# Optimization experiments

Measured on AMD Instinct MI355X. Metric: run time of the kernel, lower is better.

## Reference

```python
import jax, jax.numpy as jnp
import numpy as np
import math

_DENSE_LOCAL_W = 64
_DYADIC = [96, 128, 192, 256, 384, 512, 768, 1024, 1536]
OFFSETS = sorted(set(range(0, _DENSE_LOCAL_W + 1)) | set(_DYADIC))  # 74 offsets

B, N, D, H = 1, 2048, 1024, 16
HD = D // H


def setup_inputs() -> dict:
    key = jax.random.key(0)
    ks = jax.random.split(key, 8)
    s = 1.0 / math.sqrt(D)
    x = jax.random.normal(ks[0], (B, N, D), dtype=jnp.float32)
    Wqkv = jax.random.uniform(ks[1], (3 * D, D), jnp.float32, -s, s)
    bqkv = jax.random.uniform(ks[2], (3 * D,), jnp.float32, -s, s)
    Wgate = jax.random.uniform(ks[3], (D, D), jnp.float32, -s, s)
    bgate = jax.random.uniform(ks[4], (D,), jnp.float32, -s, s)
    Wout = jax.random.uniform(ks[5], (D, D), jnp.float32, -s, s)
    bout = jax.random.uniform(ks[6], (D,), jnp.float32, -s, s)
    # pos_bias init exactly as in the module: -log(1+delta) * alpha_h, shape (O, H)
    alphas = jnp.linspace(0.2, 2.0, H)
    deltas = jnp.array([math.log(1.0 + d) for d in OFFSETS], dtype=jnp.float32)
    pos_bias = -deltas[:, None] * alphas[None, :]
    offsets = jnp.array(OFFSETS, dtype=jnp.int32)
    return {"x": x, "Wqkv": Wqkv, "bqkv": bqkv, "Wgate": Wgate, "bgate": bgate,
            "Wout": Wout, "bout": bout, "pos_bias": pos_bias, "offsets": offsets}


def reference(x, Wqkv, bqkv, Wgate, bgate, Wout, bout, pos_bias, offsets):
    Bx, Nx, Dx = x.shape
    qkv = x @ Wqkv.T + bqkv                       # (B, N, 3D)
    q, k, v = jnp.split(qkv, 3, axis=-1)
    q = q.reshape(Bx, Nx, H, HD).transpose(0, 2, 1, 3)  # (B, H, N, HD)
    k = k.reshape(Bx, Nx, H, HD).transpose(0, 2, 1, 3)
    v = v.reshape(Bx, Nx, H, HD).transpose(0, 2, 1, 3)
    scale = HD ** -0.5

    # gather shifted K/V: position n attends to n - delta for each fixed offset
    n_idx = jnp.arange(Nx, dtype=jnp.int32)[:, None]      # (N, 1)
    idx = n_idx - offsets[None, :]                        # (N, O)
    valid = idx >= 0                                      # (N, O)
    idx_c = jnp.clip(idx, 0, Nx - 1)
    K_all = k[:, :, idx_c, :]                             # (B, H, N, O, HD)
    V_all = v[:, :, idx_c, :]

    scores = jnp.einsum('bhnd,bhnod->bhno', q, K_all) * scale
    scores = scores + pos_bias.T[None, :, None, :]        # (1, H, 1, O)
    scores = jnp.where(valid[None, None], scores, -jnp.inf)
    alpha = jax.nn.softmax(scores, axis=-1)               # (B, H, N, O)
    out = jnp.einsum('bhno,bhnod->bhnd', alpha, V_all)    # (B, H, N, HD)

    flat = out.transpose(0, 2, 1, 3).reshape(Bx, Nx, Dx)  # (B, N, D)
    gate = jax.nn.sigmoid(x @ Wgate.T + bgate)
    return (flat * gate) @ Wout.T + bout                  # dropout = identity (eval)
```

## Files before the change

### kernel.cpp

```cpp
#include <hip/hip_runtime.h>
#include <hip/hip_bf16.h>

#define SEQ_N 2048
#define DIM   1024
#define NHEAD 16
#define HDIM  64
#define LDQ   4096
#define NOFF  74
#define NDENSE 65
#define NJ    224
#define NT    16
#define PST   232
#define QST   88

typedef __attribute__((ext_vector_type(8)))  __bf16 bv8;
typedef __attribute__((ext_vector_type(4)))  __bf16 bv4;
typedef __attribute__((ext_vector_type(4)))  float  f32x4;
typedef __attribute__((ext_vector_type(16))) float  f32x16;

typedef __attribute__((address_space(3))) void as3_void;
typedef __attribute__((address_space(1))) void as1_void;

__device__ __forceinline__ void async16(const void* g, void* l) {
  __builtin_amdgcn_global_load_lds((as1_void*)(unsigned long long)g,
                                   (as3_void*)l, 16, 0, 0);
}

#define E1 (SEQ_N * DIM)
#define E2 (E1 + 3 * DIM * DIM)
#define E3 (E2 + DIM * DIM)
#define E4 (E3 + DIM * DIM)
__global__ __launch_bounds__(256) void cvt_all(
    const float* __restrict__ x, const float* __restrict__ wqkv,
    const float* __restrict__ wgate, const float* __restrict__ wout,
    __bf16* __restrict__ dst) {
  long i = ((long)blockIdx.x * 256 + threadIdx.x) * 8;
  if (i >= E4) return;
  const float* s; long o;
  if (i < E1)      { s = x;     o = i; }
  else if (i < E2) { s = wqkv;  o = i - E1; }
  else if (i < E3) { s = wgate; o = i - E2; }
  else             { s = wout;  o = i - E3; }
  float4 v0 = *(const float4*)(s + o);
  float4 v1 = *(const float4*)(s + o + 4);
  bv8 ov;
  ov[0] = (__bf16)v0.x; ov[1] = (__bf16)v0.y; ov[2] = (__bf16)v0.z; ov[3] = (__bf16)v0.w;
  ov[4] = (__bf16)v1.x; ov[5] = (__bf16)v1.y; ov[6] = (__bf16)v1.z; ov[7] = (__bf16)v1.w;
  *(bv8*)(dst + i) = ov;
}

#define BM 128
#define BKT 128

template <int BN_, typename OutT>
__global__ __launch_bounds__(256) void gemm_bt(
    const __bf16* __restrict__ A, const __bf16* __restrict__ B1,
    const __bf16* __restrict__ B2, const float* __restrict__ bias1,
    const float* __restrict__ bias2, int Nsplit,
    OutT* __restrict__ C, int ldc, int K) {
  __shared__ __attribute__((aligned(16))) __bf16 Asm[BM * BKT];
  __shared__ __attribute__((aligned(16))) __bf16 Bsm[BN_ * BKT];
  constexpr int NJ32 = BN_ / 64;
  constexpr int CA = BM * BKT / 8;
  constexpr int CB = BN_ * BKT / 8;
  constexpr int CPR = BKT / 8;

  const int tid  = threadIdx.x;
  const int lane = tid & 63;
  const int wave = tid >> 6;
  const int wr = wave >> 1, wc = wave & 1;
  const int m31 = lane & 31;
  const int h1  = lane >> 5;
  const int l7  = lane & 7;

  const int bn0 = blockIdx.x * BN_;
  const int bm0 = blockIdx.y * BM;

  const __bf16* Bp;
  const float* biasp;
  if (bn0 < Nsplit) { Bp = B1 + (size_t)bn0 * K;            biasp = bias1 + bn0; }
  else              { Bp = B2 + (size_t)(bn0 - Nsplit) * K; biasp = bias2 + (bn0 - Nsplit); }
  const __bf16* Ap = A + (size_t)bm0 * K;

  f32x16 acc[2][NJ32] = {};

  for (int kt = 0; kt < K; kt += BKT) {
    __syncthreads();
#pragma unroll
    for (int c0 = 0; c0 < CA + CB; c0 += 256) {
      int c = c0 + tid;
      if (c < CA) {
        int rr = c / CPR, qq = c % CPR;
        int qs = qq ^ (rr & 7);
        async16(Ap + (size_t)rr * K + kt + qs * 8, Asm + c * 8);
      } else {
        int cb = c - CA;
        int rr = cb / CPR, qq = cb % CPR;
        int qs = qq ^ (rr & 7);
        async16(Bp + (size_t)rr * K + kt + qs * 8, Bsm + cb * 8);
      }
    }
    __syncthreads();

#pragma unroll
    for (int kk = 0; kk < BKT / 16; ++kk) {
      const int qs = ((kk * 2 + h1) ^ l7) * 8;
      bv8 af[2], bfr[NJ32];
#pragma unroll
      for (int i = 0; i < 2; ++i)
        af[i] = *(const bv8*)(Asm + (wr * 64 + i * 32 + m31) * BKT + qs);
#pragma unroll
      for (int j = 0; j < NJ32; ++j)
        bfr[j] = *(const bv8*)(Bsm + (wc * (BN_ / 2) + j * 32 + m31) * BKT + qs);
#pragma unroll
      for (int i = 0; i < 2; ++i)
#pragma unroll
        for (int j = 0; j < NJ32; ++j)
          acc[i][j] = __builtin_amdgcn_mfma_f32_32x32x16_bf16(af[i], bfr[j], acc[i][j], 0, 0, 0);
    }
  }

#pragma unroll
  for (int i = 0; i < 2; ++i) {
#pragma unroll
    for (int j = 0; j < NJ32; ++j) {
      int ccol = wc * (BN_ / 2) + j * 32 + m31;
      float b = biasp[ccol];
#pragma unroll
      for (int reg = 0; reg < 16; ++reg) {
        int row = bm0 + wr * 64 + i * 32 + (reg & 3) + 8 * (reg >> 2) + 4 * h1;
        C[(size_t)row * ldc + bn0 + ccol] = (OutT)(acc[i][j][reg] + b);
      }
    }
  }
}

template <typename OutT>
__global__ __launch_bounds__(256) void gemm_bt64(
    const __bf16* __restrict__ A, const __bf16* __restrict__ B,
    const float* __restrict__ bias, OutT* __restrict__ C, int ldc, int K) {
  __shared__ __attribute__((aligned(16))) __bf16 Asm[64 * BKT];
  __shared__ __attribute__((aligned(16))) __bf16 Bsm[64 * BKT];
  constexpr int CM = 64 * BKT / 8;
  constexpr int CPR = BKT / 8;

  const int tid  = threadIdx.x;
  const int lane = tid & 63;
  const int wave = tid >> 6;
  const int wr = wave >> 1, wc = wave & 1;
  const int m31 = lane & 31;
  const int h1  = lane >> 5;
  const int l7  = lane & 7;

  const int bn0 = blockIdx.x * 64;
  const int bm0 = blockIdx.y * 64;

  const __bf16* Ap = A + (size_t)bm0 * K;
  const __bf16* Bp = B + (size_t)bn0 * K;
  const float* biasp = bias + bn0;

  f32x16 acc = {};

  for (int kt = 0; kt < K; kt += BKT) {
    __syncthreads();
#pragma unroll
    for (int c0 = 0; c0 < CM; c0 += 256) {
      int c = c0 + tid;
      int rr = c / CPR, qq = c % CPR;
      int qs = qq ^ (rr & 7);
      async16(Ap + (size_t)rr * K + kt + qs * 8, Asm + c * 8);
      async16(Bp + (size_t)rr * K + kt + qs * 8, Bsm + c * 8);
    }
    __syncthreads();

#pragma unroll
    for (int kk = 0; kk < BKT / 16; ++kk) {
      const int qs = ((kk * 2 + h1) ^ l7) * 8;
      bv8 a = *(const bv8*)(Asm + (wr * 32 + m31) * BKT + qs);
      bv8 b = *(const bv8*)(Bsm + (wc * 32 + m31) * BKT + qs);
      acc = __builtin_amdgcn_mfma_f32_32x32x16_bf16(a, b, acc, 0, 0, 0);
    }
  }

  {
    int ccol = wc * 32 + m31;
    float b = biasp[ccol];
#pragma unroll
    for (int reg = 0; reg < 16; ++reg) {
      int row = bm0 + wr * 32 + (reg & 3) + 8 * (reg >> 2) + 4 * h1;
      C[(size_t)row * ldc + bn0 + ccol] = (OutT)(acc[reg] + b);
    }
  }
}

__global__ __launch_bounds__(256) void attn_mfma(
    const __bf16* __restrict__ qkv,
    const float* __restrict__ pos_bias,
    const int* __restrict__ offsets,
    __bf16* __restrict__ fg) {
  const int n0 = (blockIdx.x >> 4) * NT;
  const int h  = blockIdx.x & 15;
  const int tid = threadIdx.x;
  const int lane = tid & 63;
  const int w = tid >> 6;
  const int fr = lane & 15, fq = lane >> 4;
  const int fr7 = fr & 7;

  __shared__ __attribute__((aligned(16))) __bf16 KVbuf[NJ * HDIM];
  __shared__ __attribute__((aligned(16))) __bf16 Qbuf[NT * QST];
  __shared__ __attribute__((aligned(16))) float  Sbuf[NT][80];
  __shared__ __attribute__((aligned(16))) __bf16 Pd[NT * PST];
  __shared__ float inv_l[NT];

  const int ch = lane & 7;
  const int rowin = lane >> 3;

  if (tid < 128) {
    int ni = tid >> 3, cq = tid & 7;
    bv8 q = *(const bv8*)(qkv + (size_t)(n0 + ni) * LDQ + h * HDIM + cq * 8);
    *(bv8*)(Qbuf + ni * QST + cq * 8) = q;
  }
#pragma unroll
  for (int c0 = 0; c0 < NT * PST / 8; c0 += 256) {
    int c = c0 + tid;
    if (c < NT * PST / 8) *(uint4*)(Pd + c * 8) = make_uint4(0, 0, 0, 0);
  }
  {
    int chs = ch ^ rowin;
#pragma unroll
    for (int it = 0; it < 7; ++it) {
      int jbase = it * 32 + w * 8;
      int j = jbase + rowin;
      int g;
      if (j < 80) g = n0 - 64 + j;
      else { int jj = j - 80; g = n0 - offsets[NDENSE + (jj >> 4)] + (jj & 15); }
      if (g < 0) g = 0;
      async16(qkv + (size_t)g * LDQ + DIM + h * HDIM + chs * 8,
              KVbuf + jbase * HDIM + lane * 8);
    }
  }
  __syncthreads();

  for (int jb = w; jb < 14; jb += 4) {
    f32x4 acc = {};
#pragma unroll
    for (int kk = 0; kk < 2; ++kk) {
      bv8 a = *(const bv8*)(Qbuf + fr * QST + kk * 32 + fq * 8);
      bv8 b = *(const bv8*)(KVbuf + (jb * 16 + fr) * HDIM + ((kk * 4 + fq) ^ fr7) * 8);
      acc = __builtin_amdgcn_mfma_f32_16x16x32_bf16(a, b, acc, 0, 0, 0);
    }
    int j = jb * 16 + fr;
    if (jb < 5) {
      bool gvalid = (n0 - 64 + j) >= 0;
#pragma unroll
      for (int r = 0; r < 4; ++r) {
        int ni = fq * 4 + r;
        int o = ni + 64 - j;
        if (o >= 0 && o < NDENSE)
          Sbuf[ni][o] = gvalid ? acc[r] : -3.0e38f;
      }
    } else {
      int jj = j - 80;
      int s = jj >> 4, tni = jj & 15;
      int r = tni - fq * 4;
      if (r >= 0 && r < 4) {
        bool gvalid = (n0 + tni - offsets[NDENSE + s]) >= 0;
        Sbuf[tni][NDENSE + s] = gvalid ? acc[r] : -3.0e38f;
      }
    }
  }
  __syncthreads();

  {
#pragma unroll
    for (int it = 0; it < 7; ++it) {
      int jbase = it * 32 + w * 8;
      int jv = jbase + (lane >> 5) * 4 + ((lane >> 1) & 3);
      int dv = ((lane >> 3) & 3) * 16 + (lane & 1) * 8;
      int g;
      if (jv < 80) g = n0 - 64 + jv;
      else { int jj = jv - 80; g = n0 - offsets[NDENSE + (jj >> 4)] + (jj & 15); }
      if (g < 0) g = 0;
      async16(qkv + (size_t)g * LDQ + 2 * DIM + h * HDIM + dv,
              KVbuf + jbase * HDIM + lane * 8);
    }
  }

  {
    int t = tid & 15, ni = tid >> 4;
    float sc5[5];
    float m = -3.0e38f;
#pragma unroll
    for (int k = 0; k < 5; ++k) {
      int o = t + k * 16;
      float v = -3.0e38f;
      if (o < NOFF) {
        float raw = Sbuf[ni][o];
        if (raw > -1.0e38f) v = raw * 0.125f + pos_bias[o * NHEAD + h];
      }
      sc5[k] = v;
      m = fmaxf(m, v);
    }
#pragma unroll
    for (int d = 1; d < 16; d <<= 1) m = fmaxf(m, __shfl_xor(m, d));
    float sum = 0.f;
#pragma unroll
    for (int k = 0; k < 5; ++k) {
      int o = t + k * 16;
      if (o < NOFF && sc5[k] > -1.0e38f) {
        float e = __expf(sc5[k] - m);
        sum += e;
        int j = (o < NDENSE) ? (ni + 64 - o) : (80 + (o - NDENSE) * 16 + ni);
        Pd[ni * PST + j] = (__bf16)e;
      }
    }
#pragma unroll
    for (int d = 1; d < 16; d <<= 1) sum += __shfl_xor(sum, d);
    if (t == 0) inv_l[ni] = 1.f / sum;
  }
  __syncthreads();

  {
    const int db = w;
    const unsigned vb0 = (unsigned)(size_t)(as3_void*)KVbuf
                       + fq * 1024 + db * 128 + fr * 8;
    f32x4 acc = {};
#pragma unroll
    for (int kt = 0; kt < 7; ++kt) {
      bv8 a = *(const bv8*)(Pd + fr * PST + kt * 32 + fq * 8);
      bv4 lo, hi;
      asm volatile("ds_read_b64_tr_b16 %0, %2 offset:%3\n\t"
                   "ds_read_b64_tr_b16 %1, %2 offset:%4\n\t"
                   "s_waitcnt lgkmcnt(0)"
                   : "=&v"(lo), "=&v"(hi)
                   : "v"(vb0), "i"(kt * 4096), "i"(kt * 4096 + 512));
      bv8 b;
#pragma unroll
      for (int jj = 0; jj < 4; ++jj) { b[jj] = lo[jj]; b[4 + jj] = hi[jj]; }
      acc = __builtin_amdgcn_mfma_f32_16x16x32_bf16(a, b, acc, 0, 0, 0);
    }
    int d = db * 16 + fr;
#pragma unroll
    for (int r = 0; r < 4; ++r) {
      int ni = fq * 4 + r;
      float o = acc[r] * inv_l[ni];
      float gp = (float)qkv[(size_t)(n0 + ni) * LDQ + 3 * DIM + h * HDIM + d];
      float gate = 1.f / (1.f + __expf(-gp));
      fg[(size_t)(n0 + ni) * DIM + h * HDIM + d] = (__bf16)(o * gate);
    }
  }
}

extern "C" void kernel_launch(void* const* d_in, const int* in_sizes, int n_in,
                              void* d_out, int out_size, void* d_ws, size_t ws_size,
                              hipStream_t stream) {
  const float* x        = (const float*)d_in[0];
  const float* Wqkv     = (const float*)d_in[1];
  const float* bqkv     = (const float*)d_in[2];
  const float* Wgate    = (const float*)d_in[3];
  const float* bgate    = (const float*)d_in[4];
  const float* Wout     = (const float*)d_in[5];
  const float* bout     = (const float*)d_in[6];
  const float* pos_bias = (const float*)d_in[7];
  const int*   offsets  = (const int*)d_in[8];
  float* out = (float*)d_out;

  __bf16* xb       = (__bf16*)d_ws;
  __bf16* Wqkvb    = xb    + (size_t)SEQ_N * DIM;
  __bf16* Wgateb   = Wqkvb + (size_t)3 * DIM * DIM;
  __bf16* Woutb    = Wgateb + (size_t)DIM * DIM;
  __bf16* qkvg     = Woutb + (size_t)DIM * DIM;
  __bf16* flatgate = qkvg + (size_t)SEQ_N * LDQ;

  cvt_all<<<dim3(E4 / 2048), dim3(256), 0, stream>>>(x, Wqkv, Wgate, Wout, xb);

  gemm_bt<128, __bf16><<<dim3(LDQ / 128, SEQ_N / BM), dim3(256), 0, stream>>>(
      xb, Wqkvb, Wgateb, bqkv, bgate, 3 * DIM, qkvg, LDQ, DIM);

  attn_mfma<<<dim3((SEQ_N / NT) * NHEAD), dim3(256), 0, stream>>>(
      qkvg, pos_bias, offsets, flatgate);

  gemm_bt64<float><<<dim3(DIM / 64, SEQ_N / 64), dim3(256), 0, stream>>>(
      flatgate, Woutb, bout, out, DIM, DIM);
}
```

Baseline: 142.9 us.

## Shrink QKV GEMM tiles, add occupancy hint, and remap blocks for XCD locality

Reworks the fused QKV/gate GEMM to use 64x128 tiles with a 64-deep K step, which gives 1024 workgroups instead of 512 and lets four blocks share a CU via launch bounds. Both GEMMs now remap the linear block id so that consecutive blocks on the same XCD (bid & 7) cover adjacent work tiles, with the aim of better L2 reuse of A and B rows. The price is more global-load and barrier iterations per output element and smaller per-block data reuse.

```diff
diff --git a/kernel.cpp b/kernel.cpp
--- a/kernel.cpp
+++ b/kernel.cpp
@@ -49,21 +49,19 @@
   *(bv8*)(dst + i) = ov;
 }
 
-#define BM 128
-#define BKT 128
-
-template <int BN_, typename OutT>
-__global__ __launch_bounds__(256) void gemm_bt(
+template <int BM_, int BN_, int KT, int GX, int GY, typename OutT>
+__global__ __launch_bounds__(256, 4) void gemm_bt(
     const __bf16* __restrict__ A, const __bf16* __restrict__ B1,
     const __bf16* __restrict__ B2, const float* __restrict__ bias1,
     const float* __restrict__ bias2, int Nsplit,
     OutT* __restrict__ C, int ldc, int K) {
-  __shared__ __attribute__((aligned(16))) __bf16 Asm[BM * BKT];
-  __shared__ __attribute__((aligned(16))) __bf16 Bsm[BN_ * BKT];
+  __shared__ __attribute__((aligned(16))) __bf16 Asm[BM_ * KT];
+  __shared__ __attribute__((aligned(16))) __bf16 Bsm[BN_ * KT];
+  constexpr int NI   = BM_ / 64;
   constexpr int NJ32 = BN_ / 64;
-  constexpr int CA = BM * BKT / 8;
-  constexpr int CB = BN_ * BKT / 8;
-  constexpr int CPR = BKT / 8;
+  constexpr int CA = BM_ * KT / 8;
+  constexpr int CB = BN_ * KT / 8;
+  constexpr int CPR = KT / 8;
 
   const int tid  = threadIdx.x;
   const int lane = tid & 63;
@@ -73,8 +71,11 @@
   const int h1  = lane >> 5;
   const int l7  = lane & 7;
 
-  const int bn0 = blockIdx.x * BN_;
-  const int bm0 = blockIdx.y * BM;
+  constexpr int NWG = GX * GY;
+  const int bid  = blockIdx.y * GX + blockIdx.x;
+  const int work = (bid & 7) * (NWG >> 3) + (bid >> 3);
+  const int bn0 = (work / GY) * BN_;
+  const int bm0 = (work % GY) * BM_;
 
   const __bf16* Bp;
   const float* biasp;
@@ -82,9 +83,9 @@
   else              { Bp = B2 + (size_t)(bn0 - Nsplit) * K; biasp = bias2 + (bn0 - Nsplit); }
   const __bf16* Ap = A + (size_t)bm0 * K;
 
-  f32x16 acc[2][NJ32] = {};
-
-  for (int kt = 0; kt < K; kt += BKT) {
+  f32x16 acc[NI][NJ32] = {};
+
+  for (int kt = 0; kt < K; kt += KT) {
     __syncthreads();
 #pragma unroll
     for (int c0 = 0; c0 < CA + CB; c0 += 256) {
@@ -103,17 +104,17 @@
     __syncthreads();
 
 #pragma unroll
-    for (int kk = 0; kk < BKT / 16; ++kk) {
+    for (int kk = 0; kk < KT / 16; ++kk) {
       const int qs = ((kk * 2 + h1) ^ l7) * 8;
-      bv8 af[2], bfr[NJ32];
-#pragma unroll
-      for (int i = 0; i < 2; ++i)
-        af[i] = *(const bv8*)(Asm + (wr * 64 + i * 32 + m31) * BKT + qs);
+      bv8 af[NI], bfr[NJ32];
+#pragma unroll
+      for (int i = 0; i < NI; ++i)
+        af[i] = *(const bv8*)(Asm + (wr * (BM_ / 2) + i * 32 + m31) * KT + qs);
 #pragma unroll
       for (int j = 0; j < NJ32; ++j)
-        bfr[j] = *(const bv8*)(Bsm + (wc * (BN_ / 2) + j * 32 + m31) * BKT + qs);
-#pragma unroll
-      for (int i = 0; i < 2; ++i)
+        bfr[j] = *(const bv8*)(Bsm + (wc * (BN_ / 2) + j * 32 + m31) * KT + qs);
+#pragma unroll
+      for (int i = 0; i < NI; ++i)
 #pragma unroll
         for (int j = 0; j < NJ32; ++j)
           acc[i][j] = __builtin_amdgcn_mfma_f32_32x32x16_bf16(af[i], bfr[j], acc[i][j], 0, 0, 0);
@@ -121,21 +122,23 @@
   }
 
 #pragma unroll
-  for (int i = 0; i < 2; ++i) {
+  for (int i = 0; i < NI; ++i) {
 #pragma unroll
     for (int j = 0; j < NJ32; ++j) {
       int ccol = wc * (BN_ / 2) + j * 32 + m31;
       float b = biasp[ccol];
 #pragma unroll
       for (int reg = 0; reg < 16; ++reg) {
-        int row = bm0 + wr * 64 + i * 32 + (reg & 3) + 8 * (reg >> 2) + 4 * h1;
+        int row = bm0 + wr * (BM_ / 2) + i * 32 + (reg & 3) + 8 * (reg >> 2) + 4 * h1;
         C[(size_t)row * ldc + bn0 + ccol] = (OutT)(acc[i][j][reg] + b);
       }
     }
   }
 }
 
-template <typename OutT>
+#define BKT 128
+
+template <int GX, int GY, typename OutT>
 __global__ __launch_bounds__(256) void gemm_bt64(
     const __bf16* __restrict__ A, const __bf16* __restrict__ B,
     const float* __restrict__ bias, OutT* __restrict__ C, int ldc, int K) {
@@ -152,8 +155,11 @@
   const int h1  = lane >> 5;
   const int l7  = lane & 7;
 
-  const int bn0 = blockIdx.x * 64;
-  const int bm0 = blockIdx.y * 64;
+  constexpr int NWG = GX * GY;
+  const int bid  = blockIdx.y * GX + blockIdx.x;
+  const int work = (bid & 7) * (NWG >> 3) + (bid >> 3);
+  const int bn0 = (work / GY) * 64;
+  const int bm0 = (work % GY) * 64;
 
   const __bf16* Ap = A + (size_t)bm0 * K;
   const __bf16* Bp = B + (size_t)bn0 * K;
@@ -374,12 +380,13 @@
 
   cvt_all<<<dim3(E4 / 2048), dim3(256), 0, stream>>>(x, Wqkv, Wgate, Wout, xb);
 
-  gemm_bt<128, __bf16><<<dim3(LDQ / 128, SEQ_N / BM), dim3(256), 0, stream>>>(
+  gemm_bt<64, 128, 64, 32, 32, __bf16>
+      <<<dim3(32, 32), dim3(256), 0, stream>>>(
       xb, Wqkvb, Wgateb, bqkv, bgate, 3 * DIM, qkvg, LDQ, DIM);
 
   attn_mfma<<<dim3((SEQ_N / NT) * NHEAD), dim3(256), 0, stream>>>(
       qkvg, pos_bias, offsets, flatgate);
 
-  gemm_bt64<float><<<dim3(DIM / 64, SEQ_N / 64), dim3(256), 0, stream>>>(
+  gemm_bt64<16, 32, float><<<dim3(DIM / 64, SEQ_N / 64), dim3(256), 0, stream>>>(
       flatgate, Woutb, bout, out, DIM, DIM);
 }
```

Result: no change. 144.4 us (+1.0%).
